# Performance work log

Hardware: AMD Instinct MI355X
Metric: run time of the kernel (lower is better)

The kernel has to match this reference:

```python
import jax, jax.numpy as jnp
import numpy as np

DIM = 1024
NUM_HEADS = 16
HEAD_DIM = 64
EPS = 1e-6

def setup_inputs() -> dict:
    key = jax.random.key(0)
    ks = jax.random.split(key, 6)
    x = jax.random.normal(ks[0], (4, 2048, DIM), dtype=jnp.float32)
    # Linear weights stored as (in, out); torch nn.Linear computes x @ W.T with W (out,in),
    # equivalent math with our (in,out) layout.
    Wq = jax.random.normal(ks[1], (DIM, NUM_HEADS * HEAD_DIM), dtype=jnp.float32) / np.sqrt(DIM)
    Wk = jax.random.normal(ks[2], (DIM, NUM_HEADS * HEAD_DIM), dtype=jnp.float32) / np.sqrt(DIM)
    Wv = jax.random.normal(ks[3], (DIM, NUM_HEADS * HEAD_DIM), dtype=jnp.float32) / np.sqrt(DIM)
    Wo = jax.random.normal(ks[4], (NUM_HEADS * HEAD_DIM, DIM), dtype=jnp.float32) / np.sqrt(NUM_HEADS * HEAD_DIM)
    # FeatureMap buffer: randn(head_dim, head_dim)/sqrt(head_dim)
    proj = jax.random.normal(ks[5], (HEAD_DIM, HEAD_DIM), dtype=jnp.float32) / np.sqrt(HEAD_DIM)
    return {"x": x, "Wq": Wq, "Wk": Wk, "Wv": Wv, "Wo": Wo, "proj": proj}

def _feature_map(x, proj):
    # phi(x) = elu(x @ proj) + 1  (positive features)
    return jax.nn.elu(x @ proj) + 1.0

def reference(x, Wq, Wk, Wv, Wo, proj):
    B, S, _ = x.shape
    H, D = NUM_HEADS, HEAD_DIM
    q = (x @ Wq).reshape(B, S, H, D)
    k = (x @ Wk).reshape(B, S, H, D)
    v = (x @ Wv).reshape(B, S, H, D)
    q = _feature_map(q, proj)
    k = _feature_map(k, proj)
    # scan over time: carry kv_state (B,H,D,D) and k_state (B,H,D)
    q_t = jnp.moveaxis(q, 1, 0)  # (S,B,H,D)
    k_t = jnp.moveaxis(k, 1, 0)
    v_t = jnp.moveaxis(v, 1, 0)

    def step(carry, qkv):
        kv, ksum = carry
        qt, kt, vt = qkv  # each (B,H,D)
        kv = kv + kt[..., :, None] * vt[..., None, :]  # outer product k v^T
        ksum = ksum + kt
        num = jnp.einsum('bhd,bhde->bhe', qt, kv)
        den = jnp.einsum('bhd,bhd->bh', qt, ksum) + EPS
        return (kv, ksum), num / den[..., None]

    kv0 = jnp.zeros((B, H, D, D), dtype=x.dtype)
    ks0 = jnp.zeros((B, H, D), dtype=x.dtype)
    _, out = jax.lax.scan(step, (kv0, ks0), (q_t, k_t, v_t))
    out = jnp.moveaxis(out, 0, 1).reshape(B, S, H * D)  # (B,S,H*D)
    return out @ Wo
```

## Files before the change

kernel.cpp:

```cpp
#include <hip/hip_runtime.h>

typedef unsigned short u16;
typedef unsigned int   u32;
typedef short bfrag8 __attribute__((ext_vector_type(8)));
typedef float facc4  __attribute__((ext_vector_type(4)));

#define DIM    1024
#define NH     16
#define HD     64
#define BSZ    4
#define SEQ    2048
#define MROWS  (BSZ*SEQ)
#define CHUNK  64
#define NCHUNK (SEQ/CHUNK)
#define BH     (BSZ*NH)
#define TS     72

__device__ __forceinline__ u16 f2bf(float f) {
  u32 u = __builtin_bit_cast(u32, f);
  u32 r = u + 0x7fffu + ((u >> 16) & 1u);
  return (u16)(r >> 16);
}
__device__ __forceinline__ float bf2f(u16 b) {
  return __builtin_bit_cast(float, (u32)b << 16);
}

__device__ __forceinline__ void gload_lds16(const void* g, void* l) {
  __builtin_amdgcn_global_load_lds((const __attribute__((address_space(1))) u32*)g,
                                   (__attribute__((address_space(3))) u32*)l, 16, 0, 0);
}


__global__ __launch_bounds__(256) void conv_f32_bf16(const float* __restrict__ in, u16* __restrict__ out) {
  const int i = (blockIdx.x * 256 + threadIdx.x) * 4;
  const float4 v = *(const float4*)(in + i);
  ushort4 o;
  o.x = f2bf(v.x); o.y = f2bf(v.y); o.z = f2bf(v.z); o.w = f2bf(v.w);
  *(ushort4*)(out + i) = o;
}

__global__ __launch_bounds__(256) void fold_qk(const float* __restrict__ Wq, const float* __restrict__ Wk,
                                               const float* __restrict__ proj, u16* __restrict__ wt) {
  const int i0 = blockIdx.x * 32;
  const int h  = blockIdx.y;
  const int sel = blockIdx.z;
  const float* W = sel ? Wk : Wq;
  u16* out = wt + (size_t)sel * (DIM*DIM);
  __shared__ float sp[64*64];
  __shared__ float sw[32*64];
  const int tid = threadIdx.x;
  for (int idx = tid; idx < 4096; idx += 256) sp[idx] = proj[idx];
  for (int idx = tid; idx < 2048; idx += 256) {
    int r = idx >> 6, c = idx & 63;
    sw[idx] = W[(size_t)(i0 + r)*DIM + h*64 + c];
  }
  __syncthreads();
  const int i  = tid >> 3;
  const int e0 = (tid & 7) * 8;
  #pragma unroll
  for (int ee = 0; ee < 8; ++ee) {
    const int e = e0 + ee;
    float acc = 0.f;
    for (int d = 0; d < 64; ++d) acc += sw[i*64 + d] * sp[d*64 + e];
    out[(size_t)(h*64 + e)*DIM + i0 + i] = f2bf(acc);
  }
}

__global__ __launch_bounds__(256) void trans_conv(const float* __restrict__ Wv, const float* __restrict__ Wo,
                                                  u16* __restrict__ wt) {
  const int sel = blockIdx.z;
  const float* in = sel ? Wo : Wv;
  u16* out = wt + (size_t)(2 + sel) * (DIM*DIM);
  const int n0 = blockIdx.x * 32, k0 = blockIdx.y * 32;
  __shared__ float tile[32][33];
  const int tid = threadIdx.x;
  for (int idx = tid; idx < 1024; idx += 256) {
    int r = idx >> 5, c = idx & 31;
    tile[r][c] = in[(size_t)(k0 + r)*DIM + n0 + c];
  }
  __syncthreads();
  for (int idx = tid; idx < 1024; idx += 256) {
    int r = idx >> 5, c = idx & 31;
    out[(size_t)(n0 + r)*DIM + k0 + c] = f2bf(tile[c][r]);
  }
}

template<int MODE>
__global__ __launch_bounds__(256)
void gemm_bt(const u16* __restrict__ A, const u16* __restrict__ W,
             u16* __restrict__ outb, float* __restrict__ outf) {
  __shared__ u16 lA[128*32];
  __shared__ u16 lB[128*32];
  const int tid  = threadIdx.x;
  const int wave = tid >> 6, lane = tid & 63;
  const int wm = wave >> 1, wn = wave & 1;
  const int lr = lane & 15, g = lane >> 4;

  const int m0 = blockIdx.x * 128;
  int sel, ny;
  const u16* Bt;
  if (MODE == 0) { sel = blockIdx.y >> 3; ny = blockIdx.y & 7; Bt = W + (size_t)sel * (DIM*DIM); }
  else           { sel = 0;              ny = blockIdx.y;      Bt = W; }
  const int n0 = ny * 128;

  facc4 acc[4][4] = {};

  for (int kt = 0; kt < DIM; kt += 32) {
    #pragma unroll
    for (int c = 0; c < 2; ++c) {
      const int slot = c*256 + wave*64 + lane;
      const int row  = slot >> 2, cg = slot & 3;
      const int col  = ((cg ^ (row & 3)) << 3);
      gload_lds16(A  + (size_t)(m0 + row)*DIM + kt + col, &lA[(c*256 + wave*64)*8]);
      gload_lds16(Bt + (size_t)(n0 + row)*DIM + kt + col, &lB[(c*256 + wave*64)*8]);
    }
    __syncthreads();
    bfrag8 af[4], bf[4];
    #pragma unroll
    for (int i = 0; i < 4; ++i) {
      const int ar = wm*64 + i*16 + lr;
      af[i] = *(const bfrag8*)&lA[ar*32 + ((g ^ (ar & 3)) << 3)];
      const int br = wn*64 + i*16 + lr;
      bf[i] = *(const bfrag8*)&lB[br*32 + ((g ^ (br & 3)) << 3)];
    }
    #pragma unroll
    for (int i = 0; i < 4; ++i)
      #pragma unroll
      for (int j = 0; j < 4; ++j)
        acc[i][j] = __builtin_amdgcn_mfma_f32_16x16x32_bf16(af[i], bf[j], acc[i][j], 0, 0, 0);
    __syncthreads();
  }

  const bool doElu = (MODE == 0) && (sel < 2);
  #pragma unroll
  for (int i = 0; i < 4; ++i) {
    #pragma unroll
    for (int j = 0; j < 4; ++j) {
      #pragma unroll
      for (int r = 0; r < 4; ++r) {
        const int gm = m0 + wm*64 + i*16 + g*4 + r;
        const int gn = n0 + wn*64 + j*16 + lr;
        float v = acc[i][j][r];
        if (MODE == 0) {
          if (doElu) v = (v > 0.f) ? (v + 1.f) : __expf(v);
          outb[(size_t)sel*((size_t)MROWS*DIM) + (size_t)gm*DIM + gn] = f2bf(v);
        } else {
          outf[(size_t)gm*DIM + gn] = v;
        }
      }
    }
  }
}


__global__ __launch_bounds__(256) void phaseA(const u16* __restrict__ Kb, const u16* __restrict__ Vb,
                                              u16* __restrict__ Ast, float* __restrict__ ksum) {
  const int c = blockIdx.x, bh = blockIdx.y;
  const int b = bh >> 4, h = bh & 15;
  const int tid = threadIdx.x;
  const int wave = tid >> 6, lane = tid & 63, lr = lane & 15, g = lane >> 4;
  __shared__ u16 lKt[64*TS];
  __shared__ u16 lVt[64*TS];
  const size_t mbase = (size_t)b*SEQ + (size_t)c*CHUNK;

  for (int s = tid; s < 512; s += 256) {
    const int t = s >> 3, dg = (s & 7) * 8;
    const bfrag8 kk = *(const bfrag8*)&Kb[(mbase + t)*DIM + h*64 + dg];
    const bfrag8 vv = *(const bfrag8*)&Vb[(mbase + t)*DIM + h*64 + dg];
    #pragma unroll
    for (int j = 0; j < 8; ++j) {
      lKt[(dg + j)*TS + t] = (u16)kk[j];
      lVt[(dg + j)*TS + t] = (u16)vv[j];
    }
  }
  __syncthreads();

  facc4 acc[4] = {};
  #pragma unroll
  for (int kt = 0; kt < 2; ++kt) {
    const bfrag8 af = *(const bfrag8*)&lVt[(wave*16 + lr)*TS + kt*32 + g*8];
    #pragma unroll
    for (int j = 0; j < 4; ++j) {
      const bfrag8 bk = *(const bfrag8*)&lKt[(j*16 + lr)*TS + kt*32 + g*8];
      acc[j] = __builtin_amdgcn_mfma_f32_16x16x32_bf16(af, bk, acc[j], 0, 0, 0);
    }
  }
  u16* dst = Ast + (((size_t)bh*NCHUNK + c) << 12);
  #pragma unroll
  for (int j = 0; j < 4; ++j)
    #pragma unroll
    for (int r = 0; r < 4; ++r)
      dst[(wave*16 + g*4 + r)*64 + j*16 + lr] = f2bf(acc[j][r]);

  const int d = tid >> 2, seg = tid & 3;
  const bfrag8 k0 = *(const bfrag8*)&lKt[d*TS + seg*16];
  const bfrag8 k1 = *(const bfrag8*)&lKt[d*TS + seg*16 + 8];
  float s = 0.f;
  #pragma unroll
  for (int j = 0; j < 8; ++j) s += bf2f((u16)k0[j]) + bf2f((u16)k1[j]);
  s += __shfl_xor(s, 1, 64);
  s += __shfl_xor(s, 2, 64);
  if (seg == 0) ksum[((size_t)bh*NCHUNK + c)*64 + d] = s;
}

__global__ __launch_bounds__(256) void phaseB(u16* __restrict__ Ast, float* __restrict__ ksum) {
  const int bh = blockIdx.x, slice = blockIdx.y;
  const int tid = threadIdx.x;
  u16* base = Ast + (size_t)bh*NCHUNK*4096 + slice*256 + tid;
  float v[NCHUNK];
  #pragma unroll
  for (int c = 0; c < NCHUNK; ++c) v[c] = bf2f(base[(size_t)c*4096]);
  float run = 0.f;
  #pragma unroll
  for (int c = 0; c < NCHUNK; ++c) { base[(size_t)c*4096] = f2bf(run); run += v[c]; }
  if (slice == 0 && tid < 64) {
    float rs = 0.f;
    float* kp = ksum + (size_t)bh*NCHUNK*64 + tid;
    for (int c = 0; c < NCHUNK; ++c) { const float t = kp[c*64]; kp[c*64] = rs; rs += t; }
  }
}

__global__ __launch_bounds__(256) void phaseC(const u16* __restrict__ Qb, const u16* __restrict__ Kb,
                                              const u16* __restrict__ Vb, const u16* __restrict__ Ast,
                                              const float* __restrict__ ksum, u16* __restrict__ Ob) {
  const int c = blockIdx.x, bh = blockIdx.y;
  const int b = bh >> 4, h = bh & 15;
  const int tid = threadIdx.x;
  const int wave = tid >> 6, lane = tid & 63, lr = lane & 15, g = lane >> 4;
  __shared__ u16 lS  [64*TS];
  __shared__ u16 lVt [64*TS];
  __shared__ u16 lKVt[64*TS];
  __shared__ float lks[64];
  __shared__ float lrs[64];
  __shared__ float lqk[64];
  const size_t mbase = (size_t)b*SEQ + (size_t)c*CHUNK;

  for (int s = tid; s < 512; s += 256) {
    const int t = s >> 3, dg = (s & 7) * 8;
    const bfrag8 vv = *(const bfrag8*)&Vb[(mbase + t)*DIM + h*64 + dg];
    #pragma unroll
    for (int j = 0; j < 8; ++j) lVt[(dg + j)*TS + t] = (u16)vv[j];
  }
  const u16* kvsrc = Ast + (((size_t)bh*NCHUNK + c) << 12);
  for (int s = tid; s < 512; s += 256) {
    const int e = s >> 3, dg = (s & 7) * 8;
    *(bfrag8*)&lKVt[e*TS + dg] = *(const bfrag8*)&kvsrc[e*64 + dg];
  }
  if (tid < 64) lks[tid] = ksum[((size_t)bh*NCHUNK + c)*64 + tid];

  bfrag8 qf[2], kf[4][2];
  {
    const u16* qrow = Qb + (mbase + wave*16 + lr)*DIM + h*64;
    qf[0] = *(const bfrag8*)&qrow[g*8];
    qf[1] = *(const bfrag8*)&qrow[32 + g*8];
  }
  #pragma unroll
  for (int j = 0; j < 4; ++j) {
    const u16* krow = Kb + (mbase + j*16 + lr)*DIM + h*64;
    kf[j][0] = *(const bfrag8*)&krow[g*8];
    kf[j][1] = *(const bfrag8*)&krow[32 + g*8];
  }

  facc4 accs[4] = {};
  #pragma unroll
  for (int kt = 0; kt < 2; ++kt)
    #pragma unroll
    for (int j = 0; j < 4; ++j)
      accs[j] = __builtin_amdgcn_mfma_f32_16x16x32_bf16(qf[kt], kf[j][kt], accs[j], 0, 0, 0);

  float rs[4] = {0.f, 0.f, 0.f, 0.f};
  #pragma unroll
  for (int j = 0; j < 4; ++j) {
    const int cc = j*16 + lr;
    #pragma unroll
    for (int r = 0; r < 4; ++r) {
      const int rr = wave*16 + g*4 + r;
      const float vS = (cc <= rr) ? accs[j][r] : 0.f;
      rs[r] += vS;
      lS[rr*TS + cc] = f2bf(vS);
    }
  }
  #pragma unroll
  for (int r = 0; r < 4; ++r) {
    float t = rs[r];
    t += __shfl_xor(t, 1, 64); t += __shfl_xor(t, 2, 64);
    t += __shfl_xor(t, 4, 64); t += __shfl_xor(t, 8, 64);
    if (lr == 0) lrs[wave*16 + g*4 + r] = t;
  }
  __syncthreads();

  {
    const u16* qr2 = Qb + (mbase + wave*16 + lr)*DIM + h*64 + g*16;
    const bfrag8 a0 = *(const bfrag8*)&qr2[0];
    const bfrag8 a1 = *(const bfrag8*)&qr2[8];
    float t = 0.f;
    #pragma unroll
    for (int j = 0; j < 8; ++j)
      t += bf2f((u16)a0[j]) * lks[g*16 + j] + bf2f((u16)a1[j]) * lks[g*16 + 8 + j];
    t += __shfl_xor(t, 16, 64);
    t += __shfl_xor(t, 32, 64);
    if (g == 0) lqk[wave*16 + lr] = t;
  }

  facc4 acco[4] = {};
  #pragma unroll
  for (int kt = 0; kt < 2; ++kt) {
    const bfrag8 sf = *(const bfrag8*)&lS[(wave*16 + lr)*TS + kt*32 + g*8];
    #pragma unroll
    for (int j = 0; j < 4; ++j) {
      const bfrag8 vf = *(const bfrag8*)&lVt[(j*16 + lr)*TS + kt*32 + g*8];
      acco[j] = __builtin_amdgcn_mfma_f32_16x16x32_bf16(sf, vf, acco[j], 0, 0, 0);
    }
  }
  #pragma unroll
  for (int kt = 0; kt < 2; ++kt)
    #pragma unroll
    for (int j = 0; j < 4; ++j) {
      const bfrag8 kvf = *(const bfrag8*)&lKVt[(j*16 + lr)*TS + kt*32 + g*8];
      acco[j] = __builtin_amdgcn_mfma_f32_16x16x32_bf16(qf[kt], kvf, acco[j], 0, 0, 0);
    }

  #pragma unroll
  for (int r = 0; r < 4; ++r) {
    const int rr = wave*16 + g*4 + r;
    const float rden = 1.0f / (lrs[rr] + lqk[rr] + 1e-6f);
    #pragma unroll
    for (int j = 0; j < 4; ++j)
      Ob[(mbase + rr)*DIM + h*64 + j*16 + lr] = f2bf(acco[j][r] * rden);
  }
}

extern "C" void kernel_launch(void* const* d_in, const int* in_sizes, int n_in,
                              void* d_out, int out_size, void* d_ws, size_t ws_size,
                              hipStream_t stream) {
  const float* x    = (const float*)d_in[0];
  const float* Wq   = (const float*)d_in[1];
  const float* Wk   = (const float*)d_in[2];
  const float* Wv   = (const float*)d_in[3];
  const float* Wo   = (const float*)d_in[4];
  const float* proj = (const float*)d_in[5];
  float* out = (float*)d_out;

  char* ws = (char*)d_ws;
  u16*   xb   = (u16*)  (ws);
  u16*   wt   = (u16*)  (ws + 16777216);
  u16*   qkv  = (u16*)  (ws + 25165824);
  u16*   Ob   = (u16*)  (ws + 75497472);
  u16*   Ast  = (u16*)  (ws + 92274688);
  float* ksum = (float*)(ws + 109051904);
  (void)ws_size; (void)in_sizes; (void)n_in; (void)out_size;

  conv_f32_bf16<<<dim3((MROWS*DIM)/1024), 256, 0, stream>>>(x, xb);
  fold_qk      <<<dim3(DIM/32, NH, 2), 256, 0, stream>>>(Wq, Wk, proj, wt);
  trans_conv   <<<dim3(DIM/32, DIM/32, 2), 256, 0, stream>>>(Wv, Wo, wt);

  gemm_bt<0><<<dim3(MROWS/128, 24), 256, 0, stream>>>(xb, wt, qkv, nullptr);

  const u16* Qb = qkv;
  const u16* Kb = qkv + (size_t)MROWS*DIM;
  const u16* Vb = qkv + 2*(size_t)MROWS*DIM;

  phaseA<<<dim3(NCHUNK, BH), 256, 0, stream>>>(Kb, Vb, Ast, ksum);
  phaseB<<<dim3(BH, 16), 256, 0, stream>>>(Ast, ksum);
  phaseC<<<dim3(NCHUNK, BH), 256, 0, stream>>>(Qb, Kb, Vb, Ast, ksum, Ob);

  gemm_bt<1><<<dim3(MROWS/128, 8), 256, 0, stream>>>(Ob, wt + 3*(size_t)DIM*DIM, nullptr, out);
}
```

Measured before the change: 202.5 us.

## Replace 128x128 GEMM with 256x256 tile, 4-stage LDS pipelined MFMA kernel

Rewrites the projection GEMMs as a 512-thread kernel with 256x256 output tiles and a 4-buffer LDS ring. Global-to-LDS loads run three k-steps ahead using explicit vmcnt waits and raw barriers. MFMA blocks are interleaved with fragment reads under raised wave priority, and the epilogue now writes vectorized packed stores. The aims are more data reuse per tile, load latency hidden behind compute, and fewer barrier stalls. The cost is heavier LDS use (128KB per block) and more registers, which may limit occupancy, and the hand-counted waitcnt logic is fragile.

New measurement: 205.2 us. About the same (+1.3%).

```diff
diff --git a/kernel.cpp b/kernel.cpp
--- a/kernel.cpp
+++ b/kernel.cpp
@@ -15,6 +15,9 @@
 #define NCHUNK (SEQ/CHUNK)
 #define BH     (BSZ*NH)
 #define TS     72
+#define NT     32
+
+#define BARRIER() asm volatile("s_barrier" ::: "memory")
 
 __device__ __forceinline__ u16 f2bf(float f) {
   u32 u = __builtin_bit_cast(u32, f);
@@ -86,67 +89,111 @@
 }
 
 template<int MODE>
-__global__ __launch_bounds__(256)
-void gemm_bt(const u16* __restrict__ A, const u16* __restrict__ W,
+__global__ __launch_bounds__(512, 2)
+void gemm256(const u16* __restrict__ A, const u16* __restrict__ W,
              u16* __restrict__ outb, float* __restrict__ outf) {
-  __shared__ u16 lA[128*32];
-  __shared__ u16 lB[128*32];
+  __shared__ u16 lds[4][2][256*32];
   const int tid  = threadIdx.x;
   const int wave = tid >> 6, lane = tid & 63;
-  const int wm = wave >> 1, wn = wave & 1;
+  const int wm = wave >> 2, wn = wave & 3;
   const int lr = lane & 15, g = lane >> 4;
 
-  const int m0 = blockIdx.x * 128;
-  int sel, ny;
-  const u16* Bt;
-  if (MODE == 0) { sel = blockIdx.y >> 3; ny = blockIdx.y & 7; Bt = W + (size_t)sel * (DIM*DIM); }
-  else           { sel = 0;              ny = blockIdx.y;      Bt = W; }
-  const int n0 = ny * 128;
-
-  facc4 acc[4][4] = {};
-
-  for (int kt = 0; kt < DIM; kt += 32) {
-    #pragma unroll
-    for (int c = 0; c < 2; ++c) {
-      const int slot = c*256 + wave*64 + lane;
-      const int row  = slot >> 2, cg = slot & 3;
-      const int col  = ((cg ^ (row & 3)) << 3);
-      gload_lds16(A  + (size_t)(m0 + row)*DIM + kt + col, &lA[(c*256 + wave*64)*8]);
-      gload_lds16(Bt + (size_t)(n0 + row)*DIM + kt + col, &lB[(c*256 + wave*64)*8]);
-    }
-    __syncthreads();
-    bfrag8 af[4], bf[4];
-    #pragma unroll
-    for (int i = 0; i < 4; ++i) {
-      const int ar = wm*64 + i*16 + lr;
-      af[i] = *(const bfrag8*)&lA[ar*32 + ((g ^ (ar & 3)) << 3)];
-      const int br = wn*64 + i*16 + lr;
-      bf[i] = *(const bfrag8*)&lB[br*32 + ((g ^ (br & 3)) << 3)];
-    }
-    #pragma unroll
-    for (int i = 0; i < 4; ++i)
+  const int m0 = blockIdx.x * 256;
+  int sel, n0;
+  const u16* Wt;
+  if (MODE == 0) { const int ny = blockIdx.y; sel = ny >> 2; n0 = (ny & 3) * 256; Wt = W + (size_t)sel*(DIM*DIM); }
+  else           { sel = 0; n0 = blockIdx.y * 256; Wt = W; }
+
+  auto stageX = [&](int t, int o) {
+    const int slot = o*512 + tid;
+    const int fr = slot >> 2, cg = slot & 3;
+    const int gcol = ((cg ^ ((fr >> 1) & 3)) << 3);
+    gload_lds16(A + (size_t)(m0 + fr)*DIM + t*32 + gcol,
+                &lds[t & 3][0][(o*512 + wave*64) * 8]);
+  };
+  auto stageW = [&](int t, int o) {
+    const int slot = o*512 + tid;
+    const int fr = slot >> 2, cg = slot & 3;
+    const int gcol = ((cg ^ ((fr >> 1) & 3)) << 3);
+    gload_lds16(Wt + (size_t)(n0 + fr)*DIM + t*32 + gcol,
+                &lds[t & 3][1][(o*512 + wave*64) * 8]);
+  };
+
+  #pragma unroll
+  for (int t = 0; t < 3; ++t) { stageX(t,0); stageX(t,1); stageW(t,0); stageW(t,1); }
+  asm volatile("s_waitcnt vmcnt(8)" ::: "memory");
+  BARRIER();
+
+  facc4 acc[4][8] = {};
+
+  for (int s = 0; s < NT; ++s) {
+    const int buf = s & 3;
+    const u16* lX = &lds[buf][0][0];
+    const u16* lW = &lds[buf][1][0];
+    bfrag8 wfr[4], xfr[4];
+    #pragma unroll
+    for (int wf = 0; wf < 4; ++wf) {
+      const int fr = wn*64 + wf*16 + lr;
+      wfr[wf] = *(const bfrag8*)&lW[fr*32 + ((g ^ ((fr>>1)&3)) << 3)];
+    }
+    #pragma unroll
+    for (int xf = 0; xf < 4; ++xf) {
+      const int fr = wm*128 + xf*16 + lr;
+      xfr[xf] = *(const bfrag8*)&lX[fr*32 + ((g ^ ((fr>>1)&3)) << 3)];
+    }
+    if (s + 3 < NT) { stageX(s+3, 0); stageX(s+3, 1); }
+    BARRIER();
+    __builtin_amdgcn_s_setprio(1);
+    #pragma unroll
+    for (int wf = 0; wf < 4; ++wf)
       #pragma unroll
-      for (int j = 0; j < 4; ++j)
-        acc[i][j] = __builtin_amdgcn_mfma_f32_16x16x32_bf16(af[i], bf[j], acc[i][j], 0, 0, 0);
-    __syncthreads();
+      for (int xf = 0; xf < 4; ++xf)
+        acc[wf][xf] = __builtin_amdgcn_mfma_f32_16x16x32_bf16(wfr[wf], xfr[xf], acc[wf][xf], 0, 0, 0);
+    __builtin_amdgcn_s_setprio(0);
+    BARRIER();
+    #pragma unroll
+    for (int xf = 0; xf < 4; ++xf) {
+      const int fr = wm*128 + (xf+4)*16 + lr;
+      xfr[xf] = *(const bfrag8*)&lX[fr*32 + ((g ^ ((fr>>1)&3)) << 3)];
+    }
+    if (s + 3 < NT) { stageW(s+3, 0); stageW(s+3, 1); }
+    BARRIER();
+    __builtin_amdgcn_s_setprio(1);
+    #pragma unroll
+    for (int wf = 0; wf < 4; ++wf)
+      #pragma unroll
+      for (int xf = 0; xf < 4; ++xf)
+        acc[wf][xf+4] = __builtin_amdgcn_mfma_f32_16x16x32_bf16(wfr[wf], xfr[xf], acc[wf][xf+4], 0, 0, 0);
+    __builtin_amdgcn_s_setprio(0);
+    __builtin_amdgcn_sched_barrier(0);
+    if (s <= NT-4)      asm volatile("s_waitcnt vmcnt(8)" ::: "memory");
+    else if (s == NT-3) asm volatile("s_waitcnt vmcnt(4)" ::: "memory");
+    else if (s == NT-2) asm volatile("s_waitcnt vmcnt(0)" ::: "memory");
+    if (s < NT-1) BARRIER();
   }
 
   const bool doElu = (MODE == 0) && (sel < 2);
   #pragma unroll
-  for (int i = 0; i < 4; ++i) {
-    #pragma unroll
-    for (int j = 0; j < 4; ++j) {
-      #pragma unroll
-      for (int r = 0; r < 4; ++r) {
-        const int gm = m0 + wm*64 + i*16 + g*4 + r;
-        const int gn = n0 + wn*64 + j*16 + lr;
-        float v = acc[i][j][r];
-        if (MODE == 0) {
-          if (doElu) v = (v > 0.f) ? (v + 1.f) : __expf(v);
-          outb[(size_t)sel*((size_t)MROWS*DIM) + (size_t)gm*DIM + gn] = f2bf(v);
-        } else {
-          outf[(size_t)gm*DIM + gn] = v;
+  for (int wf = 0; wf < 4; ++wf) {
+    #pragma unroll
+    for (int xf = 0; xf < 8; ++xf) {
+      const int xrow = m0 + wm*128 + xf*16 + lr;
+      const int col0 = n0 + wn*64 + wf*16 + g*4;
+      float v0 = acc[wf][xf][0], v1 = acc[wf][xf][1], v2 = acc[wf][xf][2], v3 = acc[wf][xf][3];
+      if (MODE == 0) {
+        if (doElu) {
+          v0 = (v0 > 0.f) ? (v0 + 1.f) : __expf(v0);
+          v1 = (v1 > 0.f) ? (v1 + 1.f) : __expf(v1);
+          v2 = (v2 > 0.f) ? (v2 + 1.f) : __expf(v2);
+          v3 = (v3 > 0.f) ? (v3 + 1.f) : __expf(v3);
         }
+        uint2 pk;
+        pk.x = (u32)f2bf(v0) | ((u32)f2bf(v1) << 16);
+        pk.y = (u32)f2bf(v2) | ((u32)f2bf(v3) << 16);
+        *(uint2*)&outb[(size_t)sel*((size_t)MROWS*DIM) + (size_t)xrow*DIM + col0] = pk;
+      } else {
+        float4 pk; pk.x = v0; pk.y = v1; pk.z = v2; pk.w = v3;
+        *(float4*)&outf[(size_t)xrow*DIM + col0] = pk;
       }
     }
   }
@@ -354,7 +401,7 @@
   fold_qk      <<<dim3(DIM/32, NH, 2), 256, 0, stream>>>(Wq, Wk, proj, wt);
   trans_conv   <<<dim3(DIM/32, DIM/32, 2), 256, 0, stream>>>(Wv, Wo, wt);
 
-  gemm_bt<0><<<dim3(MROWS/128, 24), 256, 0, stream>>>(xb, wt, qkv, nullptr);
+  gemm256<0><<<dim3(MROWS/256, 12), 512, 0, stream>>>(xb, wt, qkv, nullptr);
 
   const u16* Qb = qkv;
   const u16* Kb = qkv + (size_t)MROWS*DIM;
@@ -364,5 +411,5 @@
   phaseB<<<dim3(BH, 16), 256, 0, stream>>>(Ast, ksum);
   phaseC<<<dim3(NCHUNK, BH), 256, 0, stream>>>(Qb, Kb, Vb, Ast, ksum, Ob);
 
-  gemm_bt<1><<<dim3(MROWS/128, 8), 256, 0, stream>>>(Ob, wt + 3*(size_t)DIM*DIM, nullptr, out);
-}
+  gemm256<1><<<dim3(MROWS/256, 4), 512, 0, stream>>>(Ob, wt + 3*(size_t)DIM*DIM, nullptr, out);
+}
```

## Replace GEMMs with 256x256 eight-wave pipelined kernel using double-buffered LDS

Applied to the files above, without the earlier changes.

Replaces the simple 128x128 tile GEMM with a 512-thread kernel that computes 256x256 tiles over K=64 steps. It double-buffers LDS with split half-tile prefetches interleaved with MFMA quadrants, using explicit barriers, waitcnt and setprio to overlap loads with compute. Blocks are remapped across XCDs, and the epilogue uses vectorized packed stores. The gains sought are higher arithmetic intensity and latency hiding. In exchange the grid is smaller (384 and 128 blocks), which risks underfilling the 256 CUs for the output projection, and the hand-tuned synchronization is fragile.

After: 195.3 us. 3.6% less time.

```diff
diff --git a/kernel.cpp b/kernel.cpp
--- a/kernel.cpp
+++ b/kernel.cpp
@@ -15,6 +15,9 @@
 #define NCHUNK (SEQ/CHUNK)
 #define BH     (BSZ*NH)
 #define TS     72
+#define NT     16
+
+#define BARRIER() asm volatile("s_barrier" ::: "memory")
 
 __device__ __forceinline__ u16 f2bf(float f) {
   u32 u = __builtin_bit_cast(u32, f);
@@ -85,67 +88,115 @@
   }
 }
 
+#define OPENB()  { BARRIER(); asm volatile("s_waitcnt lgkmcnt(0)" ::: "memory"); __builtin_amdgcn_sched_barrier(0); }
+#define CLOSEB() { __builtin_amdgcn_sched_barrier(0); BARRIER(); }
+
+#define RD_X(MH) { _Pragma("unroll") for (int mf = 0; mf < 4; ++mf) { \
+    _Pragma("unroll") for (int kh = 0; kh < 2; ++kh) { \
+      const int row = (MH)*128 + wm*64 + mf*16 + lr; \
+      xf[mf*2+kh] = *(const bfrag8*)&lX[row*64 + (((kh*4+g) ^ (row & 7)) << 3)]; } } }
+
+#define RD_W(NHH) { _Pragma("unroll") for (int nf = 0; nf < 2; ++nf) { \
+    _Pragma("unroll") for (int kh = 0; kh < 2; ++kh) { \
+      const int row = (NHH)*128 + wn*32 + nf*16 + lr; \
+      wf[(NHH)*4 + nf*2+kh] = *(const bfrag8*)&lW[row*64 + (((kh*4+g) ^ (row & 7)) << 3)]; } } }
+
+#define MM(MH, NHH) { __builtin_amdgcn_s_setprio(1); \
+    _Pragma("unroll") for (int nf = 0; nf < 2; ++nf) { \
+    _Pragma("unroll") for (int mf = 0; mf < 4; ++mf) { \
+    _Pragma("unroll") for (int kh = 0; kh < 2; ++kh) { \
+      acc[(NHH)*2+nf][(MH)*4+mf] = __builtin_amdgcn_mfma_f32_16x16x32_bf16( \
+          wf[(NHH)*4+nf*2+kh], xf[mf*2+kh], acc[(NHH)*2+nf][(MH)*4+mf], 0, 0, 0); } } } \
+    __builtin_amdgcn_s_setprio(0); }
+
 template<int MODE>
-__global__ __launch_bounds__(256)
-void gemm_bt(const u16* __restrict__ A, const u16* __restrict__ W,
-             u16* __restrict__ outb, float* __restrict__ outf) {
-  __shared__ u16 lA[128*32];
-  __shared__ u16 lB[128*32];
+__global__ __launch_bounds__(512, 1)
+void gemm8p(const u16* __restrict__ A, const u16* __restrict__ W,
+            u16* __restrict__ outb, float* __restrict__ outf) {
+  __shared__ u16 lds[2][32768];
   const int tid  = threadIdx.x;
   const int wave = tid >> 6, lane = tid & 63;
-  const int wm = wave >> 1, wn = wave & 1;
+  const int wm = wave >> 2, wn = wave & 3;
   const int lr = lane & 15, g = lane >> 4;
 
-  const int m0 = blockIdx.x * 128;
-  int sel, ny;
-  const u16* Bt;
-  if (MODE == 0) { sel = blockIdx.y >> 3; ny = blockIdx.y & 7; Bt = W + (size_t)sel * (DIM*DIM); }
-  else           { sel = 0;              ny = blockIdx.y;      Bt = W; }
-  const int n0 = ny * 128;
-
-  facc4 acc[4][4] = {};
-
-  for (int kt = 0; kt < DIM; kt += 32) {
-    #pragma unroll
-    for (int c = 0; c < 2; ++c) {
-      const int slot = c*256 + wave*64 + lane;
-      const int row  = slot >> 2, cg = slot & 3;
-      const int col  = ((cg ^ (row & 3)) << 3);
-      gload_lds16(A  + (size_t)(m0 + row)*DIM + kt + col, &lA[(c*256 + wave*64)*8]);
-      gload_lds16(Bt + (size_t)(n0 + row)*DIM + kt + col, &lB[(c*256 + wave*64)*8]);
-    }
-    __syncthreads();
-    bfrag8 af[4], bf[4];
-    #pragma unroll
-    for (int i = 0; i < 4; ++i) {
-      const int ar = wm*64 + i*16 + lr;
-      af[i] = *(const bfrag8*)&lA[ar*32 + ((g ^ (ar & 3)) << 3)];
-      const int br = wn*64 + i*16 + lr;
-      bf[i] = *(const bfrag8*)&lB[br*32 + ((g ^ (br & 3)) << 3)];
-    }
-    #pragma unroll
-    for (int i = 0; i < 4; ++i)
+  const int NYv = (MODE == 0) ? 12 : 4;
+  const int q   = gridDim.x >> 3;
+  const int nf_ = ((int)blockIdx.x & 7) * q + ((int)blockIdx.x >> 3);
+  const int m0  = (nf_ / NYv) * 256;
+  const int ngl = (nf_ % NYv) * 256;
+
+  auto stage = [&](const u16* mat, int rowbase, int kt, int isW, int h) {
+    #pragma unroll
+    for (int o = 0; o < 2; ++o) {
+      const int s = o*512 + tid;
+      const int rih = s >> 3, sl = s & 7;
+      gload_lds16(mat + (size_t)(rowbase + h*128 + rih)*DIM + kt*64 + ((sl ^ (rih & 7)) << 3),
+                  &lds[kt & 1][isW*16384 + h*8192 + (o*512 + wave*64)*8]);
+    }
+  };
+
+  stage(A, m0, 0, 0, 0);
+  stage(W, ngl, 0, 1, 0);
+  stage(A, m0, 0, 0, 1);
+  stage(W, ngl, 0, 1, 1);
+  stage(A, m0, 1, 0, 0);
+  stage(W, ngl, 1, 1, 1);
+  asm volatile("s_waitcnt vmcnt(4)" ::: "memory");
+  BARRIER();
+
+  facc4 acc[4][8] = {};
+
+  for (int t = 0; t < NT; ++t) {
+    const u16* lX = &lds[t & 1][0];
+    const u16* lW = &lds[t & 1][16384];
+    bfrag8 xf[8], wf[8];
+    RD_X(0); RD_W(0);
+    if (t + 1 < NT) stage(A, m0, t+1, 0, 1);
+    OPENB(); MM(0,0); CLOSEB();
+    RD_W(1);
+    if (t + 1 < NT) stage(W, ngl, t+1, 1, 0);
+    OPENB(); MM(0,1); CLOSEB();
+    RD_X(1);
+    if (t + 2 < NT) stage(A, m0, t+2, 0, 0);
+    OPENB(); MM(1,1); CLOSEB();
+    if (t + 2 < NT) stage(W, ngl, t+2, 1, 1);
+    OPENB(); MM(1,0);
+    __builtin_amdgcn_sched_barrier(0);
+    if (t + 2 < NT)      asm volatile("s_waitcnt vmcnt(4)" ::: "memory");
+    else if (t + 1 < NT) asm volatile("s_waitcnt vmcnt(0)" ::: "memory");
+    if (t + 1 < NT) BARRIER();
+  }
+
+  const int sel = (MODE == 0) ? (ngl >> 10) : 0;
+  const bool doElu = (MODE == 0) && (sel < 2);
+  const int coly = (MODE == 0) ? (ngl & 1023) : ngl;
+  #pragma unroll
+  for (int nh = 0; nh < 2; ++nh) {
+    #pragma unroll
+    for (int nf = 0; nf < 2; ++nf) {
       #pragma unroll
-      for (int j = 0; j < 4; ++j)
-        acc[i][j] = __builtin_amdgcn_mfma_f32_16x16x32_bf16(af[i], bf[j], acc[i][j], 0, 0, 0);
-    __syncthreads();
-  }
-
-  const bool doElu = (MODE == 0) && (sel < 2);
-  #pragma unroll
-  for (int i = 0; i < 4; ++i) {
-    #pragma unroll
-    for (int j = 0; j < 4; ++j) {
-      #pragma unroll
-      for (int r = 0; r < 4; ++r) {
-        const int gm = m0 + wm*64 + i*16 + g*4 + r;
-        const int gn = n0 + wn*64 + j*16 + lr;
-        float v = acc[i][j][r];
-        if (MODE == 0) {
-          if (doElu) v = (v > 0.f) ? (v + 1.f) : __expf(v);
-          outb[(size_t)sel*((size_t)MROWS*DIM) + (size_t)gm*DIM + gn] = f2bf(v);
-        } else {
-          outf[(size_t)gm*DIM + gn] = v;
+      for (int mh = 0; mh < 2; ++mh) {
+        #pragma unroll
+        for (int mf = 0; mf < 4; ++mf) {
+          const facc4 a = acc[nh*2+nf][mh*4+mf];
+          const int m = m0 + mh*128 + wm*64 + mf*16 + lr;
+          const int col0 = coly + nh*128 + wn*32 + nf*16 + g*4;
+          float v0 = a[0], v1 = a[1], v2 = a[2], v3 = a[3];
+          if (MODE == 0) {
+            if (doElu) {
+              v0 = (v0 > 0.f) ? (v0 + 1.f) : __expf(v0);
+              v1 = (v1 > 0.f) ? (v1 + 1.f) : __expf(v1);
+              v2 = (v2 > 0.f) ? (v2 + 1.f) : __expf(v2);
+              v3 = (v3 > 0.f) ? (v3 + 1.f) : __expf(v3);
+            }
+            uint2 pk;
+            pk.x = (u32)f2bf(v0) | ((u32)f2bf(v1) << 16);
+            pk.y = (u32)f2bf(v2) | ((u32)f2bf(v3) << 16);
+            *(uint2*)&outb[(size_t)sel*((size_t)MROWS*DIM) + (size_t)m*DIM + col0] = pk;
+          } else {
+            float4 pk; pk.x = v0; pk.y = v1; pk.z = v2; pk.w = v3;
+            *(float4*)&outf[(size_t)m*DIM + col0] = pk;
+          }
         }
       }
     }
@@ -354,7 +405,7 @@
   fold_qk      <<<dim3(DIM/32, NH, 2), 256, 0, stream>>>(Wq, Wk, proj, wt);
   trans_conv   <<<dim3(DIM/32, DIM/32, 2), 256, 0, stream>>>(Wv, Wo, wt);
 
-  gemm_bt<0><<<dim3(MROWS/128, 24), 256, 0, stream>>>(xb, wt, qkv, nullptr);
+  gemm8p<0><<<dim3(32*12), 512, 0, stream>>>(xb, wt, qkv, nullptr);
 
   const u16* Qb = qkv;
   const u16* Kb = qkv + (size_t)MROWS*DIM;
@@ -364,5 +415,5 @@
   phaseB<<<dim3(BH, 16), 256, 0, stream>>>(Ast, ksum);
   phaseC<<<dim3(NCHUNK, BH), 256, 0, stream>>>(Qb, Kb, Vb, Ast, ksum, Ob);
 
-  gemm_bt<1><<<dim3(MROWS/128, 8), 256, 0, stream>>>(Ob, wt + 3*(size_t)DIM*DIM, nullptr, out);
-}
+  gemm8p<1><<<dim3(32*4), 512, 0, stream>>>(Ob, wt + 3*(size_t)DIM*DIM, nullptr, out);
+}
```

## Double-buffer GEMM LDS tiles, remap blocks across XCDs, vectorize epilogue stores

Applied to the files above, without the earlier changes.

Rewrites the bf16 MFMA GEMM to double-buffer the LDS tiles, so the global-to-LDS loads for the next K step are issued before the MFMAs of the current step, and the per-iteration barriers drop from two to one. Work tiles now come from a 1D grid with an XCD-aware remapping, and the swizzle, operand order and occupancy hint are adjusted. The epilogue swaps operand roles so each lane holds four consecutive columns, which lets it write packed 8-byte bf16 or 16-byte float stores. The cost is twice the LDS per block, which may limit occupancy.

New measurement: 192.7 us. 1.05x faster.

```diff
diff --git a/kernel.cpp b/kernel.cpp
--- a/kernel.cpp
+++ b/kernel.cpp
@@ -15,6 +15,7 @@
 #define NCHUNK (SEQ/CHUNK)
 #define BH     (BSZ*NH)
 #define TS     72
+#define NT32   32
 
 __device__ __forceinline__ u16 f2bf(float f) {
   u32 u = __builtin_bit_cast(u32, f);
@@ -86,67 +87,88 @@
 }
 
 template<int MODE>
-__global__ __launch_bounds__(256)
-void gemm_bt(const u16* __restrict__ A, const u16* __restrict__ W,
+__global__ __launch_bounds__(256, 3)
+void gemm128(const u16* __restrict__ A, const u16* __restrict__ W,
              u16* __restrict__ outb, float* __restrict__ outf) {
-  __shared__ u16 lA[128*32];
-  __shared__ u16 lB[128*32];
+  __shared__ u16 lds[2][2][4096];
   const int tid  = threadIdx.x;
   const int wave = tid >> 6, lane = tid & 63;
   const int wm = wave >> 1, wn = wave & 1;
   const int lr = lane & 15, g = lane >> 4;
 
-  const int m0 = blockIdx.x * 128;
-  int sel, ny;
-  const u16* Bt;
-  if (MODE == 0) { sel = blockIdx.y >> 3; ny = blockIdx.y & 7; Bt = W + (size_t)sel * (DIM*DIM); }
-  else           { sel = 0;              ny = blockIdx.y;      Bt = W; }
-  const int n0 = ny * 128;
+  const int NY  = (MODE == 0) ? 24 : 8;
+  const int q   = (int)gridDim.x >> 3;
+  const int bid = (int)blockIdx.x;
+  const int nf_ = (bid & 7) * q + (bid >> 3);
+  const int m0  = (nf_ / NY) * 128;
+  const int ngl = (nf_ % NY) * 128;
+
+  auto stage = [&](int kt) {
+    #pragma unroll
+    for (int o = 0; o < 2; ++o) {
+      const int L = o*256 + tid;
+      const int row = L >> 2, s = L & 3;
+      const int gc = ((s ^ ((row >> 1) & 3)) << 3);
+      gload_lds16(A + (size_t)(m0  + row)*DIM + kt*32 + gc, &lds[kt & 1][0][(o*256 + wave*64)*8]);
+      gload_lds16(W + (size_t)(ngl + row)*DIM + kt*32 + gc, &lds[kt & 1][1][(o*256 + wave*64)*8]);
+    }
+  };
+
+  stage(0);
+  __syncthreads();
 
   facc4 acc[4][4] = {};
 
-  for (int kt = 0; kt < DIM; kt += 32) {
-    #pragma unroll
-    for (int c = 0; c < 2; ++c) {
-      const int slot = c*256 + wave*64 + lane;
-      const int row  = slot >> 2, cg = slot & 3;
-      const int col  = ((cg ^ (row & 3)) << 3);
-      gload_lds16(A  + (size_t)(m0 + row)*DIM + kt + col, &lA[(c*256 + wave*64)*8]);
-      gload_lds16(Bt + (size_t)(n0 + row)*DIM + kt + col, &lB[(c*256 + wave*64)*8]);
-    }
+  for (int t = 0; t < NT32; ++t) {
+    if (t + 1 < NT32) stage(t + 1);
+    const u16* lX = &lds[t & 1][0][0];
+    const u16* lW = &lds[t & 1][1][0];
+    bfrag8 xf[4], wf[4];
+    #pragma unroll
+    for (int mf = 0; mf < 4; ++mf) {
+      const int row = wm*64 + mf*16 + lr;
+      xf[mf] = *(const bfrag8*)&lX[row*32 + ((g ^ ((row >> 1) & 3)) << 3)];
+    }
+    #pragma unroll
+    for (int nf = 0; nf < 4; ++nf) {
+      const int row = wn*64 + nf*16 + lr;
+      wf[nf] = *(const bfrag8*)&lW[row*32 + ((g ^ ((row >> 1) & 3)) << 3)];
+    }
+    __builtin_amdgcn_s_setprio(1);
+    #pragma unroll
+    for (int nf = 0; nf < 4; ++nf)
+      #pragma unroll
+      for (int mf = 0; mf < 4; ++mf)
+        acc[nf][mf] = __builtin_amdgcn_mfma_f32_16x16x32_bf16(wf[nf], xf[mf], acc[nf][mf], 0, 0, 0);
+    __builtin_amdgcn_s_setprio(0);
     __syncthreads();
-    bfrag8 af[4], bf[4];
-    #pragma unroll
-    for (int i = 0; i < 4; ++i) {
-      const int ar = wm*64 + i*16 + lr;
-      af[i] = *(const bfrag8*)&lA[ar*32 + ((g ^ (ar & 3)) << 3)];
-      const int br = wn*64 + i*16 + lr;
-      bf[i] = *(const bfrag8*)&lB[br*32 + ((g ^ (br & 3)) << 3)];
-    }
-    #pragma unroll
-    for (int i = 0; i < 4; ++i)
-      #pragma unroll
-      for (int j = 0; j < 4; ++j)
-        acc[i][j] = __builtin_amdgcn_mfma_f32_16x16x32_bf16(af[i], bf[j], acc[i][j], 0, 0, 0);
-    __syncthreads();
-  }
-
+  }
+
+  const int sel = (MODE == 0) ? (ngl >> 10) : 0;
   const bool doElu = (MODE == 0) && (sel < 2);
-  #pragma unroll
-  for (int i = 0; i < 4; ++i) {
-    #pragma unroll
-    for (int j = 0; j < 4; ++j) {
-      #pragma unroll
-      for (int r = 0; r < 4; ++r) {
-        const int gm = m0 + wm*64 + i*16 + g*4 + r;
-        const int gn = n0 + wn*64 + j*16 + lr;
-        float v = acc[i][j][r];
-        if (MODE == 0) {
-          if (doElu) v = (v > 0.f) ? (v + 1.f) : __expf(v);
-          outb[(size_t)sel*((size_t)MROWS*DIM) + (size_t)gm*DIM + gn] = f2bf(v);
-        } else {
-          outf[(size_t)gm*DIM + gn] = v;
+  const int coly = (MODE == 0) ? (ngl & 1023) : ngl;
+  #pragma unroll
+  for (int nf = 0; nf < 4; ++nf) {
+    #pragma unroll
+    for (int mf = 0; mf < 4; ++mf) {
+      const facc4 a = acc[nf][mf];
+      const int m = m0 + wm*64 + mf*16 + lr;
+      const int col0 = coly + wn*64 + nf*16 + g*4;
+      float v0 = a[0], v1 = a[1], v2 = a[2], v3 = a[3];
+      if (MODE == 0) {
+        if (doElu) {
+          v0 = (v0 > 0.f) ? (v0 + 1.f) : __expf(v0);
+          v1 = (v1 > 0.f) ? (v1 + 1.f) : __expf(v1);
+          v2 = (v2 > 0.f) ? (v2 + 1.f) : __expf(v2);
+          v3 = (v3 > 0.f) ? (v3 + 1.f) : __expf(v3);
         }
+        uint2 pk;
+        pk.x = (u32)f2bf(v0) | ((u32)f2bf(v1) << 16);
+        pk.y = (u32)f2bf(v2) | ((u32)f2bf(v3) << 16);
+        *(uint2*)&outb[(size_t)sel*((size_t)MROWS*DIM) + (size_t)m*DIM + col0] = pk;
+      } else {
+        float4 pk; pk.x = v0; pk.y = v1; pk.z = v2; pk.w = v3;
+        *(float4*)&outf[(size_t)m*DIM + col0] = pk;
       }
     }
   }
@@ -354,7 +376,7 @@
   fold_qk      <<<dim3(DIM/32, NH, 2), 256, 0, stream>>>(Wq, Wk, proj, wt);
   trans_conv   <<<dim3(DIM/32, DIM/32, 2), 256, 0, stream>>>(Wv, Wo, wt);
 
-  gemm_bt<0><<<dim3(MROWS/128, 24), 256, 0, stream>>>(xb, wt, qkv, nullptr);
+  gemm128<0><<<dim3(64*24), 256, 0, stream>>>(xb, wt, qkv, nullptr);
 
   const u16* Qb = qkv;
   const u16* Kb = qkv + (size_t)MROWS*DIM;
@@ -364,5 +386,5 @@
   phaseB<<<dim3(BH, 16), 256, 0, stream>>>(Ast, ksum);
   phaseC<<<dim3(NCHUNK, BH), 256, 0, stream>>>(Qb, Kb, Vb, Ast, ksum, Ob);
 
-  gemm_bt<1><<<dim3(MROWS/128, 8), 256, 0, stream>>>(Ob, wt + 3*(size_t)DIM*DIM, nullptr, out);
-}
+  gemm128<1><<<dim3(64*8), 256, 0, stream>>>(Ob, wt + 3*(size_t)DIM*DIM, nullptr, out);
+}
```
